# Kernel optimization log

Measured on AMD Instinct MI355X. Metric: run time of the kernel, lower is better.

The kernel has to match this reference:

```python
import jax, jax.numpy as jnp
import numpy as np

B, S, H = 2, 2048, 1024
NH, HD = 16, 64  # num_heads, head_dim


def setup_inputs() -> dict:
    key = jax.random.key(0)
    k1, k2, k3 = jax.random.split(key, 3)
    return {
        "hidden_states": jax.random.normal(k1, (B, S, H), dtype=jnp.float32),
        "attention_mask": jnp.zeros((B, S), dtype=jnp.float32),
        "w_qkv": jax.random.normal(k2, (3 * H, H), dtype=jnp.float32) * (1.0 / np.sqrt(H)),
        "b_qkv": jnp.zeros((3 * H,), dtype=jnp.float32),
        "w_out": jax.random.normal(k3, (H, H), dtype=jnp.float32) * (1.0 / np.sqrt(H)),
        "b_out": jnp.zeros((H,), dtype=jnp.float32),
    }


def reference(hidden_states, attention_mask, w_qkv, b_qkv, w_out, b_out):
    scale = HD ** -0.5
    qkv = hidden_states @ w_qkv.T + b_qkv          # [B,S,3H]
    qkv = qkv.reshape(B, S, 3, NH, HD)
    qkv = jnp.transpose(qkv, (2, 0, 3, 1, 4))      # [3,B,NH,S,HD]
    q, k, v = qkv[0], qkv[1], qkv[2]
    scores = jnp.einsum("bhqd,bhkd->bhqk", q, k) * scale
    # 2D additive mask broadcast to [B,1,1,S] as in torch unsqueeze path
    scores = scores + attention_mask[:, None, None, :]
    attn = jax.nn.softmax(scores, axis=-1)
    out = jnp.einsum("bhqk,bhkd->bhqd", attn, v)   # [B,NH,S,HD]
    out = jnp.transpose(out, (0, 2, 1, 3)).reshape(B, S, H)
    return out @ w_out.T + b_out
```

## Files before the change

kernel.cpp:

```cpp
#include <hip/hip_runtime.h>
#include <stdint.h>

typedef short bfrag __attribute__((ext_vector_type(8)));
typedef float f32x4 __attribute__((ext_vector_type(4)));
typedef uint  uint4v __attribute__((ext_vector_type(4)));
typedef uint  uint2v __attribute__((ext_vector_type(2)));

#define LOG2E 1.4426950408889634f
#define SWZ(row) ((((row) & 3) | (((row) >> 1) & 4)) << 4)

__device__ __forceinline__ ushort f2bf(float x){
  union { float f; uint32_t u; } c; c.f = x;
  uint32_t r = (c.u + 0x7fffu + ((c.u >> 16) & 1u)) >> 16;
  return (ushort)r;
}

__device__ __forceinline__ uint32_t cvt_pk_bf16(float lo, float hi){
  uint32_t r;
  asm("v_cvt_pk_bf16_f32 %0, %1, %2" : "=v"(r) : "v"(lo), "v"(hi));
  return r;
}

__device__ __forceinline__ float redq_max(float x){
  x = fmaxf(x, __shfl_xor(x, 16));
  x = fmaxf(x, __shfl_xor(x, 32));
  return x;
}
__device__ __forceinline__ float redq_sum(float x){
  x += __shfl_xor(x, 16);
  x += __shfl_xor(x, 32);
  return x;
}

__device__ __forceinline__ void load_lds16(const void* g, void* l){
  __builtin_amdgcn_global_load_lds((const __attribute__((address_space(1))) void*)g,
                                   (__attribute__((address_space(3))) void*)l,
                                   16, 0, 0);
}

__global__ void cast_all(const float* __restrict__ hs, const float* __restrict__ wqkv,
                         const float* __restrict__ wout, const float* __restrict__ mask,
                         ushort* __restrict__ out, float* __restrict__ mask2){
  const int i = blockIdx.x * blockDim.x + threadIdx.x;
  if (i < 2097152){
    float4 f;
    if (i < 1048576)       f = ((const float4*)hs)[i];
    else if (i < 1835008)  f = ((const float4*)wqkv)[i - 1048576];
    else                   f = ((const float4*)wout)[i - 1835008];
    ushort4 u;
    u.x = f2bf(f.x); u.y = f2bf(f.y); u.z = f2bf(f.z); u.w = f2bf(f.w);
    ((ushort4*)out)[i] = u;
  } else {
    const int j = i - 2097152;
    float4 m = ((const float4*)mask)[j];
    m.x *= LOG2E; m.y *= LOG2E; m.z *= LOG2E; m.w *= LOG2E;
    ((float4*)mask2)[j] = m;
  }
}

__global__ __launch_bounds__(256)
void transpose_v(const ushort* __restrict__ v, ushort* __restrict__ vt){
  __shared__ ushort T[64*64];
  const int t = threadIdx.x;
  const int bh = blockIdx.y, s0 = blockIdx.x * 64;
  const ushort* vb = v + ((size_t)bh * 2048 + s0) * 64;
  ushort* vtb = vt + (size_t)bh * 64 * 2048 + s0;
#pragma unroll
  for (int i = 0; i < 2; i++){
    const int s = (t >> 3) + i*32, c = (t & 7) * 8;
    bfrag x = *(const bfrag*)(vb + (size_t)s * 64 + c);
    *(bfrag*)((char*)T + ((s*128 + c*2) ^ (((s >> 3) & 7) << 4))) = x;
  }
  __syncthreads();
#pragma unroll
  for (int i = 0; i < 2; i++){
    const int d = (t >> 3) + i*32, c = (t & 7) * 8;
    bfrag y;
#pragma unroll
    for (int j = 0; j < 8; j++){
      const int s = c + j;
      y[j] = *(const ushort*)((char*)T + ((s*128 + d*2) ^ (((s >> 3) & 7) << 4)));
    }
    *(bfrag*)(vtb + (size_t)d * 2048 + c) = y;
  }
}

template<int EPI>
__global__ __launch_bounds__(256)
void gemm_bt(const ushort* __restrict__ A, const ushort* __restrict__ B,
             const float* __restrict__ bias,
             ushort* __restrict__ dq, ushort* __restrict__ dk, ushort* __restrict__ dv,
             float* __restrict__ dout,
             int M, int N, int K)
{
  __shared__ ushort Alds[2][128*32];
  __shared__ ushort Blds[2][128*32];
  const int t = threadIdx.x;
  const int w = t >> 6, l = t & 63;
  const int lr = l & 15, lg = l >> 4;
  const int m0 = blockIdx.x * 128, n0 = blockIdx.y * 128;
  const int wm = (w >> 1) * 64, wn = (w & 1) * 64;

  f32x4 acc[4][4] = {};

  auto stage = [&](int buf, int kt){
#pragma unroll
    for (int i = 0; i < 2; i++){
      const int row = i*64 + w*16 + (l >> 2);
      const int ce  = (l & 3) * 8;
      load_lds16(A + (size_t)(m0 + row) * K + kt*32 + ce, &Alds[buf][(i*64 + w*16) * 32]);
      load_lds16(B + (size_t)(n0 + row) * K + kt*32 + ce, &Blds[buf][(i*64 + w*16) * 32]);
    }
  };

  const int nk = K >> 5;
  int cur = 0;
  stage(0, 0);
  __syncthreads();
  for (int kt = 0; kt < nk; kt++){
    if (kt + 1 < nk) stage(cur ^ 1, kt + 1);
    bfrag af[4], bfv[4];
#pragma unroll
    for (int f = 0; f < 4; f++){
      af[f]  = *(const bfrag*)&Alds[cur][(wm + f*16 + lr) * 32 + lg * 8];
      bfv[f] = *(const bfrag*)&Blds[cur][(wn + f*16 + lr) * 32 + lg * 8];
    }
#pragma unroll
    for (int mf = 0; mf < 4; mf++)
#pragma unroll
      for (int nf = 0; nf < 4; nf++)
        acc[mf][nf] = __builtin_amdgcn_mfma_f32_16x16x32_bf16(af[mf], bfv[nf], acc[mf][nf], 0, 0, 0);
    __syncthreads();
    cur ^= 1;
  }

#pragma unroll
  for (int mf = 0; mf < 4; mf++){
#pragma unroll
    for (int nf = 0; nf < 4; nf++){
      const int col = n0 + wn + nf*16 + lr;
      const float bs = bias[col];
#pragma unroll
      for (int r = 0; r < 4; r++){
        const int row = m0 + wm + mf*16 + lg*4 + r;
        const float vv = acc[mf][nf][r] + bs;
        if (EPI == 1){
          const int which = col >> 10;
          const int hd = col & 1023;
          const int bb = row >> 11, s = row & 2047;
          const int bh = (bb << 4) + (hd >> 6);
          ushort* dst = (which == 0) ? dq : (which == 1) ? dk : dv;
          dst[((size_t)bh * 2048 + s) * 64 + (hd & 63)] = f2bf(vv);
        } else {
          dout[(size_t)row * N + col] = vv;
        }
      }
    }
  }
}

__global__ __launch_bounds__(512, 4)
void flash_attn(const ushort* __restrict__ q, const ushort* __restrict__ k,
                const ushort* __restrict__ vt, const float* __restrict__ mask2,
                ushort* __restrict__ ao)
{
  __shared__ ushort Klds[2][64*64];
  __shared__ ushort Vlds[2][64*64];
  const int t = threadIdx.x;
  const int w = t >> 6, l = t & 63;
  const int lr = l & 15, lg = l >> 4;
  const int bh = blockIdx.y;
  const int b = bh >> 4, h = bh & 15;
  const int q0 = blockIdx.x * 128;
  const ushort* qb  = q  + (size_t)bh * 2048 * 64;
  const ushort* kb  = k  + (size_t)bh * 2048 * 64;
  const ushort* vtb = vt + (size_t)bh * 64 * 2048;
  const float* mb = mask2 + b * 2048;

  const int srow = t >> 3;
  const int soff = ((t & 7) * 16) ^ SWZ(srow);

  auto stageKV = [&](int buf, int kv0){
    load_lds16((const char*)(kb + (size_t)kv0 * 64) + srow*128 + soff,
               (char*)&Klds[buf][0] + w*1024);
    load_lds16((const char*)vtb + (size_t)srow * 4096 + kv0*2 + soff,
               (char*)&Vlds[buf][0] + w*1024);
  };

  bfrag qf[2];
#pragma unroll
  for (int kf = 0; kf < 2; kf++){
    const int row = q0 + w*16 + lr;
    qf[kf] = *(const bfrag*)(qb + (size_t)row * 64 + kf*32 + lg*8);
  }

  float mrun = -1e30f, lsum = 0.f;
  f32x4 oacc[4] = {};

  const float SC2 = 0.125f * LOG2E;
  const int rbase = (lr >> 2) * 8 + (lr & 3);

  stageKV(0, 0);

  int cur = 0;
  for (int kv0 = 0; kv0 < 2048; kv0 += 64){
    __syncthreads();
    if (kv0 + 64 < 2048) stageKV(cur ^ 1, kv0 + 64);

    float4 mk[4];
#pragma unroll
    for (int nf = 0; nf < 4; nf++)
      mk[nf] = *(const float4*)(mb + kv0 + ((nf & 1) << 5) + (lg << 3) + ((nf >> 1) << 2));

    bfrag bk[4][2];
#pragma unroll
    for (int nf = 0; nf < 4; nf++){
      const int rho = ((nf & 1) << 5) + ((nf >> 1) << 2) + rbase;
      const int rsw = SWZ(rho);
#pragma unroll
      for (int kf = 0; kf < 2; kf++){
        const int kbyte = kf*64 + lg*16;
        bk[nf][kf] = *(const bfrag*)((const char*)&Klds[cur][0] + rho*128 + (kbyte ^ rsw));
      }
    }
    f32x4 sa[4] = {};
#pragma unroll
    for (int nf = 0; nf < 4; nf++)
#pragma unroll
      for (int kf = 0; kf < 2; kf++)
        sa[nf] = __builtin_amdgcn_mfma_f32_16x16x32_bf16(bk[nf][kf], qf[kf], sa[nf], 0, 0, 0);

    float sc[4][4];
#pragma unroll
    for (int nf = 0; nf < 4; nf++){
      sc[nf][0] = fmaf(sa[nf][0], SC2, mk[nf].x);
      sc[nf][1] = fmaf(sa[nf][1], SC2, mk[nf].y);
      sc[nf][2] = fmaf(sa[nf][2], SC2, mk[nf].z);
      sc[nf][3] = fmaf(sa[nf][3], SC2, mk[nf].w);
    }
    float mx = sc[0][0];
#pragma unroll
    for (int nf = 0; nf < 4; nf++)
#pragma unroll
      for (int r = 0; r < 4; r++) mx = fmaxf(mx, sc[nf][r]);

    if (__any(mx > mrun + 8.f)){
      const float mnew = fmaxf(mrun, redq_max(mx));
      const float c = __builtin_amdgcn_exp2f(mrun - mnew);
      mrun = mnew;
      lsum *= c;
#pragma unroll
      for (int nf = 0; nf < 4; nf++) oacc[nf] *= c;
    }

    float p[4][4];
    float ps = 0.f;
#pragma unroll
    for (int nf = 0; nf < 4; nf++)
#pragma unroll
      for (int r = 0; r < 4; r++){
        p[nf][r] = __builtin_amdgcn_exp2f(sc[nf][r] - mrun);
        ps += p[nf][r];
      }
    lsum += ps;

    bfrag ap[2];
#pragma unroll
    for (int kf = 0; kf < 2; kf++){
      uint4v tv = { cvt_pk_bf16(p[kf][0],   p[kf][1]),
                    cvt_pk_bf16(p[kf][2],   p[kf][3]),
                    cvt_pk_bf16(p[kf+2][0], p[kf+2][1]),
                    cvt_pk_bf16(p[kf+2][2], p[kf+2][3]) };
      ap[kf] = __builtin_bit_cast(bfrag, tv);
    }

    bfrag bv[4][2];
#pragma unroll
    for (int nf = 0; nf < 4; nf++)
#pragma unroll
      for (int kf = 0; kf < 2; kf++){
        const int d = nf*16 + lr;
        const int kbyte = kf*64 + lg*16;
        bv[nf][kf] = *(const bfrag*)((const char*)&Vlds[cur][0] + d*128 + (kbyte ^ SWZ(d)));
      }
#pragma unroll
    for (int nf = 0; nf < 4; nf++)
#pragma unroll
      for (int kf = 0; kf < 2; kf++)
        oacc[nf] = __builtin_amdgcn_mfma_f32_16x16x32_bf16(bv[nf][kf], ap[kf], oacc[nf], 0, 0, 0);

    cur ^= 1;
  }

  const float inv = 1.f / redq_sum(lsum);
  ushort* orow = ao + (size_t)(b*2048 + q0 + w*16 + lr) * 1024 + h*64 + lg*4;
#pragma unroll
  for (int nf = 0; nf < 4; nf++){
    const uint32_t w01 = cvt_pk_bf16(oacc[nf][0] * inv, oacc[nf][1] * inv);
    const uint32_t w23 = cvt_pk_bf16(oacc[nf][2] * inv, oacc[nf][3] * inv);
    uint2v vv = {w01, w23};
    *(uint2v*)(orow + nf*16) = vv;
  }
}

extern "C" void kernel_launch(void* const* d_in, const int* in_sizes, int n_in,
                              void* d_out, int out_size, void* d_ws, size_t ws_size,
                              hipStream_t stream)
{
  (void)in_sizes; (void)n_in; (void)out_size; (void)ws_size;
  const float* hs   = (const float*)d_in[0];
  const float* mask = (const float*)d_in[1];
  const float* wqkv = (const float*)d_in[2];
  const float* bqkv = (const float*)d_in[3];
  const float* wout = (const float*)d_in[4];
  const float* bout = (const float*)d_in[5];
  float* out = (float*)d_out;

  char* ws = (char*)d_ws;
  ushort* hs_bf = (ushort*)(ws);
  ushort* w1_bf = (ushort*)(ws + 8388608);
  ushort* w2_bf = (ushort*)(ws + 14680064);
  ushort* q_bf  = (ushort*)(ws + 16777216);
  ushort* k_bf  = (ushort*)(ws + 25165824);
  ushort* v_bf  = (ushort*)(ws + 33554432);
  ushort* vt_bf = (ushort*)(ws + 41943040);
  ushort* ao_bf = (ushort*)(ws + 50331648);
  float*  mask2 = (float*)(ws + 58720256);

  cast_all<<<8196, 256, 0, stream>>>(hs, wqkv, wout, mask, (ushort*)ws, mask2);

  gemm_bt<1><<<dim3(32, 24), 256, 0, stream>>>(hs_bf, w1_bf, bqkv,
                                               q_bf, k_bf, v_bf, nullptr,
                                               4096, 3072, 1024);
  transpose_v<<<dim3(32, 32), 256, 0, stream>>>(v_bf, vt_bf);
  flash_attn<<<dim3(16, 32), 512, 0, stream>>>(q_bf, k_bf, vt_bf, mask2, ao_bf);
  gemm_bt<2><<<dim3(32, 8), 256, 0, stream>>>(ao_bf, w2_bf, bout,
                                              nullptr, nullptr, nullptr, out,
                                              4096, 1024, 1024);
}
```

Baseline: 128.6 us.

## Fuse V transpose into QKV GEMM epilogue and double query rows per wave

The QKV GEMM epilogue now writes V directly in transposed [bh, d, s] layout using packed bf16 stores, which removes the separate transpose_v kernel launch and its extra pass over V. The flash attention kernel switches to 256 threads, with each wave handling two 16-row query groups, so every K/V fragment read from LDS feeds twice as many MFMAs. Each thread now stages two rows of K and V per tile. The cost is higher register pressure from the doubled accumulators, plus fewer waves per block to hide latency.

```diff
diff --git a/kernel.cpp b/kernel.cpp
--- a/kernel.cpp
+++ b/kernel.cpp
@@ -58,38 +58,11 @@
   }
 }
 
-__global__ __launch_bounds__(256)
-void transpose_v(const ushort* __restrict__ v, ushort* __restrict__ vt){
-  __shared__ ushort T[64*64];
-  const int t = threadIdx.x;
-  const int bh = blockIdx.y, s0 = blockIdx.x * 64;
-  const ushort* vb = v + ((size_t)bh * 2048 + s0) * 64;
-  ushort* vtb = vt + (size_t)bh * 64 * 2048 + s0;
-#pragma unroll
-  for (int i = 0; i < 2; i++){
-    const int s = (t >> 3) + i*32, c = (t & 7) * 8;
-    bfrag x = *(const bfrag*)(vb + (size_t)s * 64 + c);
-    *(bfrag*)((char*)T + ((s*128 + c*2) ^ (((s >> 3) & 7) << 4))) = x;
-  }
-  __syncthreads();
-#pragma unroll
-  for (int i = 0; i < 2; i++){
-    const int d = (t >> 3) + i*32, c = (t & 7) * 8;
-    bfrag y;
-#pragma unroll
-    for (int j = 0; j < 8; j++){
-      const int s = c + j;
-      y[j] = *(const ushort*)((char*)T + ((s*128 + d*2) ^ (((s >> 3) & 7) << 4)));
-    }
-    *(bfrag*)(vtb + (size_t)d * 2048 + c) = y;
-  }
-}
-
 template<int EPI>
 __global__ __launch_bounds__(256)
 void gemm_bt(const ushort* __restrict__ A, const ushort* __restrict__ B,
              const float* __restrict__ bias,
-             ushort* __restrict__ dq, ushort* __restrict__ dk, ushort* __restrict__ dv,
+             ushort* __restrict__ dq, ushort* __restrict__ dk, ushort* __restrict__ dvt,
              float* __restrict__ dout,
              int M, int N, int K)
 {
@@ -140,26 +113,34 @@
     for (int nf = 0; nf < 4; nf++){
       const int col = n0 + wn + nf*16 + lr;
       const float bs = bias[col];
-#pragma unroll
-      for (int r = 0; r < 4; r++){
-        const int row = m0 + wm + mf*16 + lg*4 + r;
-        const float vv = acc[mf][nf][r] + bs;
-        if (EPI == 1){
-          const int which = col >> 10;
-          const int hd = col & 1023;
-          const int bb = row >> 11, s = row & 2047;
-          const int bh = (bb << 4) + (hd >> 6);
-          ushort* dst = (which == 0) ? dq : (which == 1) ? dk : dv;
-          dst[((size_t)bh * 2048 + s) * 64 + (hd & 63)] = f2bf(vv);
+      if (EPI == 1){
+        const int which = col >> 10;
+        const int hd = col & 1023;
+        const int bh = ((m0 >> 11) << 4) + (hd >> 6);
+        const int s0 = (m0 + wm + mf*16 + lg*4) & 2047;
+        if (which == 2){
+          const float v0 = acc[mf][nf][0] + bs, v1 = acc[mf][nf][1] + bs;
+          const float v2 = acc[mf][nf][2] + bs, v3 = acc[mf][nf][3] + bs;
+          uint2v pv = { cvt_pk_bf16(v0, v1), cvt_pk_bf16(v2, v3) };
+          *(uint2v*)(dvt + ((size_t)bh * 64 + (hd & 63)) * 2048 + s0) = pv;
         } else {
-          dout[(size_t)row * N + col] = vv;
+          ushort* dst = (which == 0) ? dq : dk;
+#pragma unroll
+          for (int r = 0; r < 4; r++)
+            dst[((size_t)bh * 2048 + s0 + r) * 64 + (hd & 63)] = f2bf(acc[mf][nf][r] + bs);
         }
-      }
-    }
-  }
-}
-
-__global__ __launch_bounds__(512, 4)
+      } else {
+#pragma unroll
+        for (int r = 0; r < 4; r++){
+          const int row = m0 + wm + mf*16 + lg*4 + r;
+          dout[(size_t)row * N + col] = acc[mf][nf][r] + bs;
+        }
+      }
+    }
+  }
+}
+
+__global__ __launch_bounds__(256, 2)
 void flash_attn(const ushort* __restrict__ q, const ushort* __restrict__ k,
                 const ushort* __restrict__ vt, const float* __restrict__ mask2,
                 ushort* __restrict__ ao)
@@ -177,25 +158,32 @@
   const ushort* vtb = vt + (size_t)bh * 64 * 2048;
   const float* mb = mask2 + b * 2048;
 
-  const int srow = t >> 3;
-  const int soff = ((t & 7) * 16) ^ SWZ(srow);
+  const int srow0 = t >> 3;
+  const int scol  = (t & 7) * 16;
 
   auto stageKV = [&](int buf, int kv0){
-    load_lds16((const char*)(kb + (size_t)kv0 * 64) + srow*128 + soff,
-               (char*)&Klds[buf][0] + w*1024);
-    load_lds16((const char*)vtb + (size_t)srow * 4096 + kv0*2 + soff,
-               (char*)&Vlds[buf][0] + w*1024);
+#pragma unroll
+    for (int i = 0; i < 2; i++){
+      const int row = srow0 + i*32;
+      const int off = scol ^ SWZ(row);
+      load_lds16((const char*)(kb + (size_t)kv0 * 64) + row*128 + off,
+                 (char*)&Klds[buf][0] + i*4096 + w*1024);
+      load_lds16((const char*)vtb + (size_t)row * 4096 + kv0*2 + off,
+                 (char*)&Vlds[buf][0] + i*4096 + w*1024);
+    }
   };
 
-  bfrag qf[2];
-#pragma unroll
-  for (int kf = 0; kf < 2; kf++){
-    const int row = q0 + w*16 + lr;
-    qf[kf] = *(const bfrag*)(qb + (size_t)row * 64 + kf*32 + lg*8);
-  }
-
-  float mrun = -1e30f, lsum = 0.f;
-  f32x4 oacc[4] = {};
+  bfrag qf[2][2];
+#pragma unroll
+  for (int qg = 0; qg < 2; qg++)
+#pragma unroll
+    for (int kf = 0; kf < 2; kf++){
+      const int row = q0 + w*32 + qg*16 + lr;
+      qf[qg][kf] = *(const bfrag*)(qb + (size_t)row * 64 + kf*32 + lg*8);
+    }
+
+  float mrun[2] = {-1e30f, -1e30f}, lsum[2] = {0.f, 0.f};
+  f32x4 oacc[2][4] = {};
 
   const float SC2 = 0.125f * LOG2E;
   const int rbase = (lr >> 2) * 8 + (lr & 3);
@@ -223,55 +211,66 @@
         bk[nf][kf] = *(const bfrag*)((const char*)&Klds[cur][0] + rho*128 + (kbyte ^ rsw));
       }
     }
-    f32x4 sa[4] = {};
-#pragma unroll
-    for (int nf = 0; nf < 4; nf++)
-#pragma unroll
-      for (int kf = 0; kf < 2; kf++)
-        sa[nf] = __builtin_amdgcn_mfma_f32_16x16x32_bf16(bk[nf][kf], qf[kf], sa[nf], 0, 0, 0);
-
-    float sc[4][4];
-#pragma unroll
-    for (int nf = 0; nf < 4; nf++){
-      sc[nf][0] = fmaf(sa[nf][0], SC2, mk[nf].x);
-      sc[nf][1] = fmaf(sa[nf][1], SC2, mk[nf].y);
-      sc[nf][2] = fmaf(sa[nf][2], SC2, mk[nf].z);
-      sc[nf][3] = fmaf(sa[nf][3], SC2, mk[nf].w);
-    }
-    float mx = sc[0][0];
-#pragma unroll
-    for (int nf = 0; nf < 4; nf++)
-#pragma unroll
-      for (int r = 0; r < 4; r++) mx = fmaxf(mx, sc[nf][r]);
-
-    if (__any(mx > mrun + 8.f)){
-      const float mnew = fmaxf(mrun, redq_max(mx));
-      const float c = __builtin_amdgcn_exp2f(mrun - mnew);
-      mrun = mnew;
-      lsum *= c;
-#pragma unroll
-      for (int nf = 0; nf < 4; nf++) oacc[nf] *= c;
-    }
-
-    float p[4][4];
-    float ps = 0.f;
-#pragma unroll
-    for (int nf = 0; nf < 4; nf++)
-#pragma unroll
-      for (int r = 0; r < 4; r++){
-        p[nf][r] = __builtin_amdgcn_exp2f(sc[nf][r] - mrun);
-        ps += p[nf][r];
-      }
-    lsum += ps;
-
-    bfrag ap[2];
-#pragma unroll
-    for (int kf = 0; kf < 2; kf++){
-      uint4v tv = { cvt_pk_bf16(p[kf][0],   p[kf][1]),
-                    cvt_pk_bf16(p[kf][2],   p[kf][3]),
-                    cvt_pk_bf16(p[kf+2][0], p[kf+2][1]),
-                    cvt_pk_bf16(p[kf+2][2], p[kf+2][3]) };
-      ap[kf] = __builtin_bit_cast(bfrag, tv);
+    f32x4 sa[2][4] = {};
+#pragma unroll
+    for (int qg = 0; qg < 2; qg++)
+#pragma unroll
+      for (int nf = 0; nf < 4; nf++)
+#pragma unroll
+        for (int kf = 0; kf < 2; kf++)
+          sa[qg][nf] = __builtin_amdgcn_mfma_f32_16x16x32_bf16(bk[nf][kf], qf[qg][kf], sa[qg][nf], 0, 0, 0);
+
+    float sc[2][4][4], mx[2];
+#pragma unroll
+    for (int qg = 0; qg < 2; qg++){
+#pragma unroll
+      for (int nf = 0; nf < 4; nf++){
+        sc[qg][nf][0] = fmaf(sa[qg][nf][0], SC2, mk[nf].x);
+        sc[qg][nf][1] = fmaf(sa[qg][nf][1], SC2, mk[nf].y);
+        sc[qg][nf][2] = fmaf(sa[qg][nf][2], SC2, mk[nf].z);
+        sc[qg][nf][3] = fmaf(sa[qg][nf][3], SC2, mk[nf].w);
+      }
+      float m01 = fmaxf(fmaxf(sc[qg][0][0], sc[qg][0][1]), fmaxf(sc[qg][0][2], sc[qg][0][3]));
+#pragma unroll
+      for (int nf = 1; nf < 4; nf++)
+#pragma unroll
+        for (int r = 0; r < 4; r++) m01 = fmaxf(m01, sc[qg][nf][r]);
+      mx[qg] = m01;
+    }
+
+    const bool grew = (mx[0] > mrun[0] + 8.f) | (mx[1] > mrun[1] + 8.f);
+    if (__any(grew)){
+#pragma unroll
+      for (int qg = 0; qg < 2; qg++){
+        const float mnew = fmaxf(mrun[qg], redq_max(mx[qg]));
+        const float c = __builtin_amdgcn_exp2f(mrun[qg] - mnew);
+        mrun[qg] = mnew;
+        lsum[qg] *= c;
+#pragma unroll
+        for (int nf = 0; nf < 4; nf++) oacc[qg][nf] *= c;
+      }
+    }
+
+    bfrag ap[2][2];
+#pragma unroll
+    for (int qg = 0; qg < 2; qg++){
+      float ps = 0.f;
+#pragma unroll
+      for (int nf = 0; nf < 4; nf++)
+#pragma unroll
+        for (int r = 0; r < 4; r++){
+          sc[qg][nf][r] = __builtin_amdgcn_exp2f(sc[qg][nf][r] - mrun[qg]);
+          ps += sc[qg][nf][r];
+        }
+      lsum[qg] += ps;
+#pragma unroll
+      for (int kf = 0; kf < 2; kf++){
+        uint4v tv = { cvt_pk_bf16(sc[qg][kf][0],   sc[qg][kf][1]),
+                      cvt_pk_bf16(sc[qg][kf][2],   sc[qg][kf][3]),
+                      cvt_pk_bf16(sc[qg][kf+2][0], sc[qg][kf+2][1]),
+                      cvt_pk_bf16(sc[qg][kf+2][2], sc[qg][kf+2][3]) };
+        ap[qg][kf] = __builtin_bit_cast(bfrag, tv);
+      }
     }
 
     bfrag bv[4][2];
@@ -284,22 +283,27 @@
         bv[nf][kf] = *(const bfrag*)((const char*)&Vlds[cur][0] + d*128 + (kbyte ^ SWZ(d)));
       }
 #pragma unroll
-    for (int nf = 0; nf < 4; nf++)
-#pragma unroll
-      for (int kf = 0; kf < 2; kf++)
-        oacc[nf] = __builtin_amdgcn_mfma_f32_16x16x32_bf16(bv[nf][kf], ap[kf], oacc[nf], 0, 0, 0);
+    for (int qg = 0; qg < 2; qg++)
+#pragma unroll
+      for (int nf = 0; nf < 4; nf++)
+#pragma unroll
+        for (int kf = 0; kf < 2; kf++)
+          oacc[qg][nf] = __builtin_amdgcn_mfma_f32_16x16x32_bf16(bv[nf][kf], ap[qg][kf], oacc[qg][nf], 0, 0, 0);
 
     cur ^= 1;
   }
 
-  const float inv = 1.f / redq_sum(lsum);
-  ushort* orow = ao + (size_t)(b*2048 + q0 + w*16 + lr) * 1024 + h*64 + lg*4;
-#pragma unroll
-  for (int nf = 0; nf < 4; nf++){
-    const uint32_t w01 = cvt_pk_bf16(oacc[nf][0] * inv, oacc[nf][1] * inv);
-    const uint32_t w23 = cvt_pk_bf16(oacc[nf][2] * inv, oacc[nf][3] * inv);
-    uint2v vv = {w01, w23};
-    *(uint2v*)(orow + nf*16) = vv;
+#pragma unroll
+  for (int qg = 0; qg < 2; qg++){
+    const float inv = 1.f / redq_sum(lsum[qg]);
+    ushort* orow = ao + (size_t)(b*2048 + q0 + w*32 + qg*16 + lr) * 1024 + h*64 + lg*4;
+#pragma unroll
+    for (int nf = 0; nf < 4; nf++){
+      const uint32_t w01 = cvt_pk_bf16(oacc[qg][nf][0] * inv, oacc[qg][nf][1] * inv);
+      const uint32_t w23 = cvt_pk_bf16(oacc[qg][nf][2] * inv, oacc[qg][nf][3] * inv);
+      uint2v vv = {w01, w23};
+      *(uint2v*)(orow + nf*16) = vv;
+    }
   }
 }
 
@@ -322,18 +326,16 @@
   ushort* w2_bf = (ushort*)(ws + 14680064);
   ushort* q_bf  = (ushort*)(ws + 16777216);
   ushort* k_bf  = (ushort*)(ws + 25165824);
-  ushort* v_bf  = (ushort*)(ws + 33554432);
-  ushort* vt_bf = (ushort*)(ws + 41943040);
-  ushort* ao_bf = (ushort*)(ws + 50331648);
-  float*  mask2 = (float*)(ws + 58720256);
+  ushort* vt_bf = (ushort*)(ws + 33554432);
+  ushort* ao_bf = (ushort*)(ws + 41943040);
+  float*  mask2 = (float*)(ws + 50331648);
 
   cast_all<<<8196, 256, 0, stream>>>(hs, wqkv, wout, mask, (ushort*)ws, mask2);
 
   gemm_bt<1><<<dim3(32, 24), 256, 0, stream>>>(hs_bf, w1_bf, bqkv,
-                                               q_bf, k_bf, v_bf, nullptr,
+                                               q_bf, k_bf, vt_bf, nullptr,
                                                4096, 3072, 1024);
-  transpose_v<<<dim3(32, 32), 256, 0, stream>>>(v_bf, vt_bf);
-  flash_attn<<<dim3(16, 32), 512, 0, stream>>>(q_bf, k_bf, vt_bf, mask2, ao_bf);
+  flash_attn<<<dim3(16, 32), 256, 0, stream>>>(q_bf, k_bf, vt_bf, mask2, ao_bf);
   gemm_bt<2><<<dim3(32, 8), 256, 0, stream>>>(ao_bf, w2_bf, bout,
                                               nullptr, nullptr, nullptr, out,
                                               4096, 1024, 1024);
```

Result: no change. 127.8 us (-0.6%).
